# Optimization experiments

Hardware: AMD Instinct MI355X
Metric: run time of the kernel (lower is better)

The kernel has to match this reference:

```python
import jax, jax.numpy as jnp
import numpy as np

BLOCK_M, BLOCK_K = 16, 64
THRES = 0.8


def setup_inputs() -> dict:
    key = jax.random.key(0)
    kx, kw = jax.random.split(key)
    bsz, seq, in_f, out_f = 128, 1, 4096, 11008
    x = jax.random.normal(kx, (bsz, seq, in_f), dtype=jnp.float16)
    # kaiming_uniform_(a=sqrt(5)) on a (in,out) weight -> bound = 1/sqrt(fan_in)
    bound = 1.0 / np.sqrt(in_f)
    weight = jax.random.uniform(kw, (in_f, out_f), dtype=jnp.float16,
                                minval=-bound, maxval=bound)
    bias = jnp.zeros((out_f,), dtype=jnp.float16)
    return {"x": x, "weight": weight, "bias": bias}


def reference(x, weight, bias):
    bsz, seq, hidden = x.shape
    x2 = x.reshape(bsz * seq, hidden)          # (M, K), seq == 1 decode path
    M, K = x2.shape
    # avg_magnitude_threshold: per (BLOCK_M, BLOCK_K) block mean |x| vs thres
    blocks = x2.reshape(M // BLOCK_M, BLOCK_M, K // BLOCK_K, BLOCK_K)
    avg = jnp.mean(jnp.abs(blocks).astype(jnp.float32), axis=(1, 3))  # (M/bm, K/bk)
    mask = avg > THRES                           # block active if avg magnitude above thres
    # blocksparse_masked_gemm: skipped blocks contribute nothing -> zero them out
    xm = jnp.where(mask[:, None, :, None], blocks, jnp.float16(0)).reshape(M, K)
    y = xm @ weight                              # (M, out_features)
    return y.reshape(bsz, seq, -1) + bias
```

## Files before the change

### kernel.cpp

```cpp
#include <hip/hip_runtime.h>
#include <stdint.h>

using f32x4   = __attribute__((ext_vector_type(4))) float;
using short8  = __attribute__((ext_vector_type(8))) short;
using float4v = __attribute__((ext_vector_type(4))) float;
using float2v = __attribute__((ext_vector_type(2))) float;
using uint2v  = __attribute__((ext_vector_type(2))) unsigned int;
using uint4v  = __attribute__((ext_vector_type(4))) unsigned int;

#define NCOL 11008
#define KDIM 4096
#define LSTRIDE 264

__device__ __forceinline__ unsigned pk_bf16(float a, float b) {
  unsigned ua = __float_as_uint(a); ua += 0x7fffu + ((ua >> 16) & 1u);
  unsigned ub = __float_as_uint(b); ub += 0x7fffu + ((ub >> 16) & 1u);
  return (ua >> 16) | (ub & 0xffff0000u);
}

__global__ __launch_bounds__(256) void mask_convert_kernel(
    const float* __restrict__ x, unsigned* __restrict__ xbf) {
  const int rb = blockIdx.x;
  const int g  = blockIdx.y;
  const int t  = threadIdx.x;
  __shared__ double part[256];
  __shared__ unsigned sh_bits;

  const float* base = x + (size_t)rb * 16 * KDIM + g * 512 + t * 2;
  double s = 0.0;
#pragma unroll
  for (int r = 0; r < 16; ++r) {
    float2v a = *(const float2v*)(base + (size_t)r * KDIM);
    s += (double)fabsf(a[0]) + (double)fabsf(a[1]);
  }
  part[t] = s;
  __syncthreads();
  if (t < 8) {
    double acc = 0.0;
#pragma unroll
    for (int u = 0; u < 32; ++u) acc += part[t * 32 + u];
    bool on = (acc * (1.0 / 1024.0)) > (double)0.8f;
    unsigned long long bal = __ballot(on);
    if (t == 0) sh_bits = (unsigned)(bal & 0xffu);
  }
  __syncthreads();
  const unsigned keep = (sh_bits >> (t >> 5)) & 1u;

  unsigned* dst = xbf + (size_t)rb * 16 * (KDIM / 2) + g * 256 + t;
#pragma unroll
  for (int r = 0; r < 16; ++r) {
    float2v a = *(const float2v*)(base + (size_t)r * KDIM);
    dst[(size_t)r * (KDIM / 2)] = keep ? pk_bf16(a[0], a[1]) : 0u;
  }
}

__global__ __launch_bounds__(256) void gemm_kernel(
    const unsigned* __restrict__ xbf, const float* __restrict__ w,
    const float* __restrict__ bias, float* __restrict__ out) {

  __shared__ __align__(16) uint8_t lds[64 * LSTRIDE];

  const int tid  = threadIdx.x;
  const int lane = tid & 63;
  const int wv   = tid >> 6;
  const int c    = lane & 15;
  const int q    = lane >> 4;
  const int n0   = blockIdx.x * 128;
  const int kz   = blockIdx.y;

  f32x4 acc[8][2] = {};

  const int sk = tid >> 5;
  const int sn = (tid & 31) * 4;
  uint8_t* wS = lds + (size_t)sk * LSTRIDE + sn * 2;

  float4v wr[8];
#define ISSUE_W(KB)                                                      \
  {                                                                      \
    const float* wp = w + (size_t)(kz * 512 + (KB)*64 + sk) * NCOL + n0 + sn; \
    _Pragma("unroll")                                                    \
    for (int r = 0; r < 8; ++r)                                          \
      wr[r] = *(const float4v*)(wp + (size_t)r * 8 * NCOL);              \
  }

  const uint4v* aBase = (const uint4v*)xbf + (size_t)c * 512 + kz * 64 + q;

  ISSUE_W(0);
  for (int kb = 0; kb < 8; ++kb) {
    __syncthreads();
#pragma unroll
    for (int r = 0; r < 8; ++r) {
      uint2v v;
      v[0] = pk_bf16(wr[r][0], wr[r][1]);
      v[1] = pk_bf16(wr[r][2], wr[r][3]);
      *(uint2v*)(wS + (size_t)r * 8 * LSTRIDE) = v;
    }
    __syncthreads();
    if (kb < 7) ISSUE_W(kb + 1);

#pragma unroll
    for (int ks = 0; ks < 2; ++ks) {
      union { uint4v u; short8 v; } am[8];
#pragma unroll
      for (int mt = 0; mt < 8; ++mt)
        am[mt].u = aBase[(size_t)mt * 16 * 512 + kb * 8 + ks * 4];

      const uint8_t* wb = lds + (size_t)(ks * 32 + q * 8) * LSTRIDE + (wv * 32 + 2 * c) * 2;
      unsigned wj[8];
#pragma unroll
      for (int j = 0; j < 8; ++j)
        wj[j] = *(const unsigned*)(wb + (size_t)j * LSTRIDE);
      union { short8 v; unsigned u[4]; } be, bo;
#pragma unroll
      for (int p = 0; p < 4; ++p) {
        be.u[p] = (wj[2 * p] & 0x0000ffffu) | (wj[2 * p + 1] << 16);
        bo.u[p] = (wj[2 * p] >> 16) | (wj[2 * p + 1] & 0xffff0000u);
      }
#pragma unroll
      for (int mt = 0; mt < 8; ++mt) {
        acc[mt][0] = __builtin_amdgcn_mfma_f32_16x16x32_bf16(am[mt].v, be.v, acc[mt][0], 0, 0, 0);
        acc[mt][1] = __builtin_amdgcn_mfma_f32_16x16x32_bf16(am[mt].v, bo.v, acc[mt][1], 0, 0, 0);
      }
    }
  }
#undef ISSUE_W

  const int colE = n0 + wv * 32 + 2 * c;
  const float bE = (kz == 0) ? bias[colE] : 0.f;
  const float bO = (kz == 0) ? bias[colE + 1] : 0.f;
#pragma unroll
  for (int mt = 0; mt < 8; ++mt) {
#pragma unroll
    for (int p = 0; p < 4; ++p) {
      const int row = mt * 16 + q * 4 + p;
      float* o = out + (size_t)row * NCOL + colE;
      unsafeAtomicAdd(o,     acc[mt][0][p] + bE);
      unsafeAtomicAdd(o + 1, acc[mt][1][p] + bO);
    }
  }
}

extern "C" void kernel_launch(void* const* d_in, const int* in_sizes, int n_in,
                              void* d_out, int out_size, void* d_ws, size_t ws_size,
                              hipStream_t stream) {
  const float* x    = (const float*)d_in[0];
  const float* w    = (const float*)d_in[1];
  const float* bias = (const float*)d_in[2];
  float* out        = (float*)d_out;
  unsigned* xbf     = (unsigned*)d_ws;

  hipLaunchKernelGGL(mask_convert_kernel, dim3(8, 8), dim3(256), 0, stream, x, xbf);
  hipMemsetAsync(out, 0, (size_t)out_size * sizeof(float), stream);
  hipLaunchKernelGGL(gemm_kernel, dim3(86, 8), dim3(256), 0, stream,
                     xbf, w, bias, out);
}
```

Measured before the change: 329.9 us.

## Halve GEMM column tile and replace atomic split-K with partial-sum reduce kernel

The GEMM tile narrows from 128 to 64 columns, with waves arranged 2x2 over M and N, so the grid doubles to 172x8 blocks for better occupancy across CUs. Each block now writes its split-K partial to a workspace buffer instead of atomically adding into the output. A separate reduce kernel sums the 8 partials and adds the bias, which also removes the output memset. The weight staging is reorganised into wider contiguous row loads and 16-byte LDS stores. The cost is extra workspace traffic: roughly 45MB of fp32 partials written and then read back, plus one more kernel launch.

Result: faster. 296.0 us (-10.3%).

```diff
diff --git a/kernel.cpp b/kernel.cpp
--- a/kernel.cpp
+++ b/kernel.cpp
@@ -5,12 +5,11 @@
 using short8  = __attribute__((ext_vector_type(8))) short;
 using float4v = __attribute__((ext_vector_type(4))) float;
 using float2v = __attribute__((ext_vector_type(2))) float;
-using uint2v  = __attribute__((ext_vector_type(2))) unsigned int;
 using uint4v  = __attribute__((ext_vector_type(4))) unsigned int;
 
 #define NCOL 11008
 #define KDIM 4096
-#define LSTRIDE 264
+#define LSTR 136
 
 __device__ __forceinline__ unsigned pk_bf16(float a, float b) {
   unsigned ua = __float_as_uint(a); ua += 0x7fffu + ((ua >> 16) & 1u);
@@ -56,60 +55,71 @@
 
 __global__ __launch_bounds__(256) void gemm_kernel(
     const unsigned* __restrict__ xbf, const float* __restrict__ w,
-    const float* __restrict__ bias, float* __restrict__ out) {
+    float* __restrict__ pws) {
 
-  __shared__ __align__(16) uint8_t lds[64 * LSTRIDE];
+  __shared__ __align__(16) uint8_t lds[64 * LSTR];
 
   const int tid  = threadIdx.x;
   const int lane = tid & 63;
   const int wv   = tid >> 6;
+  const int wm   = wv >> 1;
+  const int wn   = wv & 1;
   const int c    = lane & 15;
   const int q    = lane >> 4;
-  const int n0   = blockIdx.x * 128;
+  const int n0   = blockIdx.x * 64;
   const int kz   = blockIdx.y;
 
-  f32x4 acc[8][2] = {};
+  f32x4 acc[4][2] = {};
 
-  const int sk = tid >> 5;
-  const int sn = (tid & 31) * 4;
-  uint8_t* wS = lds + (size_t)sk * LSTRIDE + sn * 2;
+  const int sr = tid >> 2, g4 = tid & 3;
+  const float* wBase = w + (size_t)(kz * 512 + sr) * NCOL + n0 + g4 * 16;
+  uint8_t* wS = lds + (size_t)sr * LSTR + g4 * 32;
 
-  float4v wr[8];
-#define ISSUE_W(KB)                                                      \
-  {                                                                      \
-    const float* wp = w + (size_t)(kz * 512 + (KB)*64 + sk) * NCOL + n0 + sn; \
-    _Pragma("unroll")                                                    \
-    for (int r = 0; r < 8; ++r)                                          \
-      wr[r] = *(const float4v*)(wp + (size_t)r * 8 * NCOL);              \
+  float4v wr0, wr1, wr2, wr3;
+#define ISSUE_W(KB)                                                     \
+  {                                                                     \
+    const float* wp = wBase + (size_t)(KB) * 64 * NCOL;                 \
+    wr0 = *(const float4v*)(wp);                                        \
+    wr1 = *(const float4v*)(wp + 4);                                    \
+    wr2 = *(const float4v*)(wp + 8);                                    \
+    wr3 = *(const float4v*)(wp + 12);                                   \
   }
 
-  const uint4v* aBase = (const uint4v*)xbf + (size_t)c * 512 + kz * 64 + q;
+  const uint4v* aBase = (const uint4v*)xbf +
+                        ((size_t)(wm * 64 + c)) * (KDIM / 8) + kz * 64 + q;
 
   ISSUE_W(0);
   for (int kb = 0; kb < 8; ++kb) {
     __syncthreads();
-#pragma unroll
-    for (int r = 0; r < 8; ++r) {
-      uint2v v;
-      v[0] = pk_bf16(wr[r][0], wr[r][1]);
-      v[1] = pk_bf16(wr[r][2], wr[r][3]);
-      *(uint2v*)(wS + (size_t)r * 8 * LSTRIDE) = v;
+    {
+      uint4v v;
+      v[0] = pk_bf16(wr0[0], wr0[1]);
+      v[1] = pk_bf16(wr0[2], wr0[3]);
+      v[2] = pk_bf16(wr1[0], wr1[1]);
+      v[3] = pk_bf16(wr1[2], wr1[3]);
+      *(uint4v*)(wS) = v;
+      uint4v u;
+      u[0] = pk_bf16(wr2[0], wr2[1]);
+      u[1] = pk_bf16(wr2[2], wr2[3]);
+      u[2] = pk_bf16(wr3[0], wr3[1]);
+      u[3] = pk_bf16(wr3[2], wr3[3]);
+      *(uint4v*)(wS + 16) = u;
     }
     __syncthreads();
     if (kb < 7) ISSUE_W(kb + 1);
 
 #pragma unroll
     for (int ks = 0; ks < 2; ++ks) {
-      union { uint4v u; short8 v; } am[8];
+      union { uint4v u; short8 v; } am[4];
 #pragma unroll
-      for (int mt = 0; mt < 8; ++mt)
-        am[mt].u = aBase[(size_t)mt * 16 * 512 + kb * 8 + ks * 4];
+      for (int mt = 0; mt < 4; ++mt)
+        am[mt].u = aBase[(size_t)mt * 16 * (KDIM / 8) + kb * 8 + ks * 4];
 
-      const uint8_t* wb = lds + (size_t)(ks * 32 + q * 8) * LSTRIDE + (wv * 32 + 2 * c) * 2;
+      const uint8_t* wb = lds + (size_t)(ks * 32 + q * 8) * LSTR + (wn * 32 + 2 * c) * 2;
       unsigned wj[8];
 #pragma unroll
       for (int j = 0; j < 8; ++j)
-        wj[j] = *(const unsigned*)(wb + (size_t)j * LSTRIDE);
+        wj[j] = *(const unsigned*)(wb + (size_t)j * LSTR);
       union { short8 v; unsigned u[4]; } be, bo;
 #pragma unroll
       for (int p = 0; p < 4; ++p) {
@@ -117,7 +127,7 @@
         bo.u[p] = (wj[2 * p] >> 16) | (wj[2 * p + 1] & 0xffff0000u);
       }
 #pragma unroll
-      for (int mt = 0; mt < 8; ++mt) {
+      for (int mt = 0; mt < 4; ++mt) {
         acc[mt][0] = __builtin_amdgcn_mfma_f32_16x16x32_bf16(am[mt].v, be.v, acc[mt][0], 0, 0, 0);
         acc[mt][1] = __builtin_amdgcn_mfma_f32_16x16x32_bf16(am[mt].v, bo.v, acc[mt][1], 0, 0, 0);
       }
@@ -125,19 +135,40 @@
   }
 #undef ISSUE_W
 
-  const int colE = n0 + wv * 32 + 2 * c;
-  const float bE = (kz == 0) ? bias[colE] : 0.f;
-  const float bO = (kz == 0) ? bias[colE + 1] : 0.f;
+  float* P = pws + ((size_t)blockIdx.x * 8 + kz) * (128 * 64);
+  const int colL = wn * 32 + 2 * c;
 #pragma unroll
-  for (int mt = 0; mt < 8; ++mt) {
+  for (int mt = 0; mt < 4; ++mt) {
 #pragma unroll
     for (int p = 0; p < 4; ++p) {
-      const int row = mt * 16 + q * 4 + p;
-      float* o = out + (size_t)row * NCOL + colE;
-      unsafeAtomicAdd(o,     acc[mt][0][p] + bE);
-      unsafeAtomicAdd(o + 1, acc[mt][1][p] + bO);
+      const int row = wm * 64 + mt * 16 + q * 4 + p;
+      float2v st;
+      st[0] = acc[mt][0][p];
+      st[1] = acc[mt][1][p];
+      *(float2v*)(P + (size_t)row * 64 + colL) = st;
     }
   }
+}
+
+__global__ __launch_bounds__(256) void reduce_kernel(
+    const float* __restrict__ pws, const float* __restrict__ bias,
+    float* __restrict__ out) {
+  const int idx = blockIdx.x * 256 + threadIdx.x;
+  const int c2  = idx & 31;
+  const int r   = (idx >> 5) & 127;
+  const int nt  = idx >> 12;
+  const float* p = pws + (size_t)nt * 8 * (128 * 64) + (size_t)r * 64 + c2 * 2;
+  float s0 = 0.f, s1 = 0.f;
+#pragma unroll
+  for (int z = 0; z < 8; ++z) {
+    float2v v = *(const float2v*)(p + (size_t)z * (128 * 64));
+    s0 += v[0]; s1 += v[1];
+  }
+  const int col = nt * 64 + c2 * 2;
+  float2v o;
+  o[0] = s0 + bias[col];
+  o[1] = s1 + bias[col + 1];
+  *(float2v*)(out + (size_t)r * NCOL + col) = o;
 }
 
 extern "C" void kernel_launch(void* const* d_in, const int* in_sizes, int n_in,
@@ -148,9 +179,9 @@
   const float* bias = (const float*)d_in[2];
   float* out        = (float*)d_out;
   unsigned* xbf     = (unsigned*)d_ws;
+  float* pws        = (float*)((char*)d_ws + (1u << 20));
 
   hipLaunchKernelGGL(mask_convert_kernel, dim3(8, 8), dim3(256), 0, stream, x, xbf);
-  hipMemsetAsync(out, 0, (size_t)out_size * sizeof(float), stream);
-  hipLaunchKernelGGL(gemm_kernel, dim3(86, 8), dim3(256), 0, stream,
-                     xbf, w, bias, out);
+  hipLaunchKernelGGL(gemm_kernel, dim3(172, 8), dim3(256), 0, stream, xbf, w, pws);
+  hipLaunchKernelGGL(reduce_kernel, dim3(2752), dim3(256), 0, stream, pws, bias, out);
 }
```
